# Performance work log

Measured on AMD Instinct MI355X. Metric: run time of the kernel, lower is better.

## Reference

```python
import jax, jax.numpy as jnp
import numpy as np

N_TOKEN = 267735
CUTS = [0, 20000, 40000, 200000, 267735]
DIV = 4
D_MODEL = 1024
N_HEAD = 16
D_HEAD = 64
D_INNER = 4096
N_LAYER = 4
QLEN = 512
MLEN = 512
BSZ = 4
EPS = 1e-5


def _ln(x, g, b):
    mu = jnp.mean(x, axis=-1, keepdims=True)
    var = jnp.var(x, axis=-1, keepdims=True)
    return (x - mu) * jax.lax.rsqrt(var + EPS) * g + b


def _rel_shift(x):
    # x: [qlen, klen, bsz, n_head]
    q, k, b, n = x.shape
    x = jnp.pad(x, ((0, 0), (1, 0), (0, 0), (0, 0)))
    x = x.reshape(k + 1, q, b, n)[1:]
    return x.reshape(q, k, b, n)


def setup_inputs() -> dict:
    key = jax.random.key(0)
    ks = list(jax.random.split(key, 32))
    p = lambda i, shape: 0.02 * jax.random.normal(ks[i], shape, dtype=jnp.float32)
    inp = {}
    inp['input_ids'] = jax.random.randint(ks[0], (BSZ, QLEN), 0, N_TOKEN, dtype=jnp.int32)
    inp['mems'] = 0.05 * jax.random.normal(ks[1], (N_LAYER, MLEN, BSZ, D_MODEL), dtype=jnp.float32)
    # adaptive embedding: cluster tables + projections (div_val=4)
    for i in range(4):
        l, r = CUTS[i], CUTS[i + 1]
        d_i = D_MODEL // (DIV ** i)
        inp[f'emb{i}'] = p(2 + i, (r - l, d_i))
        inp[f'proj{i}'] = p(6 + i, (d_i, D_MODEL))
    H = N_HEAD * D_HEAD
    inp['qkv_W'] = p(10, (N_LAYER, D_MODEL, 3 * H))
    inp['r_W'] = p(11, (N_LAYER, D_MODEL, H))
    inp['o_W'] = p(12, (N_LAYER, H, D_MODEL))
    inp['r_w_bias'] = p(13, (N_LAYER, N_HEAD, D_HEAD))
    inp['r_r_bias'] = p(14, (N_LAYER, N_HEAD, D_HEAD))
    inp['ln1_g'] = jnp.ones((N_LAYER, D_MODEL), jnp.float32)
    inp['ln1_b'] = jnp.zeros((N_LAYER, D_MODEL), jnp.float32)
    inp['ff_w1'] = p(15, (N_LAYER, D_MODEL, D_INNER))
    inp['ff_b1'] = jnp.zeros((N_LAYER, D_INNER), jnp.float32)
    inp['ff_w2'] = p(16, (N_LAYER, D_INNER, D_MODEL))
    inp['ff_b2'] = jnp.zeros((N_LAYER, D_MODEL), jnp.float32)
    inp['ln2_g'] = jnp.ones((N_LAYER, D_MODEL), jnp.float32)
    inp['ln2_b'] = jnp.zeros((N_LAYER, D_MODEL), jnp.float32)
    return inp


def _forward(input_ids, mems, embs, projs, qkv_W, r_W, o_W, r_w_bias, r_r_bias,
             ln1_g, ln1_b, ff_w1, ff_b1, ff_w2, ff_b2, ln2_g, ln2_b):
    ids = input_ids.T  # [qlen, bsz]
    qlen, bsz = ids.shape
    mems = jax.lax.stop_gradient(mems)  # mems are detached in the original
    mlen = mems.shape[1]
    klen = qlen + mlen

    # --- adaptive embedding (masked gather + scatter-add, same math as boolean_mask/scatter_nd) ---
    flat = ids.reshape(-1)
    emb = jnp.zeros((flat.shape[0], D_MODEL), jnp.float32)
    for i in range(4):
        l, r = CUTS[i], CUTS[i + 1]
        mask = (flat >= l) & (flat < r)
        idx = jnp.clip(flat - l, 0, r - l - 1)
        e_i = jnp.einsum('id,de->ie', embs[i][idx], projs[i])
        emb = emb + jnp.where(mask[:, None], e_i, 0.0)
    word_emb = (emb * (D_MODEL ** 0.5)).reshape(qlen, bsz, D_MODEL)

    # --- sinusoidal relative positions, pos_seq = klen-1 .. 0 ---
    pos_seq = jnp.arange(klen - 1, -1, -1, dtype=jnp.float32)
    inv_freq = 1.0 / (10000.0 ** (jnp.arange(0, D_MODEL, 2, dtype=jnp.float32) / D_MODEL))
    sinusoid = jnp.einsum('i,j->ij', pos_seq, inv_freq)
    pos_emb = jnp.concatenate([jnp.sin(sinusoid), jnp.cos(sinusoid)], axis=-1)  # [klen, d_model]

    # causal mask over memory-extended keys: [qlen, klen]
    attn_mask = jnp.triu(jnp.ones((qlen, klen), jnp.float32), k=1 + mlen)
    mask4 = attn_mask[:, :, None, None]
    scale = 1.0 / (D_HEAD ** 0.5)

    h = word_emb
    for l in range(N_LAYER):
        cat = jnp.concatenate([mems[l], h], axis=0)  # [klen, bsz, d_model]
        w_heads = jnp.einsum('kbd,dh->kbh', cat, qkv_W[l])
        r_head_k = jnp.einsum('kd,dh->kh', pos_emb, r_W[l]).reshape(klen, N_HEAD, D_HEAD)
        q_h, k_h, v_h = jnp.split(w_heads, 3, axis=-1)
        q_h = q_h[-qlen:].reshape(qlen, bsz, N_HEAD, D_HEAD)
        k_h = k_h.reshape(klen, bsz, N_HEAD, D_HEAD)
        v_h = v_h.reshape(klen, bsz, N_HEAD, D_HEAD)
        AC = jnp.einsum('ibnd,jbnd->ijbn', q_h + r_w_bias[l], k_h)
        BD = _rel_shift(jnp.einsum('ibnd,jnd->ijbn', q_h + r_r_bias[l], r_head_k))
        score = (AC + BD) * scale
        score = score * (1.0 - mask4) - 1e30 * mask4
        prob = jax.nn.softmax(score, axis=1)
        attn_vec = jnp.einsum('ijbn,jbnd->ibnd', prob, v_h).reshape(qlen, bsz, N_HEAD * D_HEAD)
        attn_out = jnp.einsum('ibh,hd->ibd', attn_vec, o_W[l])
        h = _ln(h + attn_out, ln1_g[l], ln1_b[l])
        ff = jnp.einsum('ibf,fd->ibd', jax.nn.relu(jnp.einsum('ibd,df->ibf', h, ff_w1[l]) + ff_b1[l]), ff_w2[l]) + ff_b2[l]
        h = _ln(h + ff, ln2_g[l], ln2_b[l])

    return h.transpose(1, 0, 2)  # [bsz, qlen, d_model]


def reference(input_ids, mems, emb0, emb1, emb2, emb3, proj0, proj1, proj2, proj3,
              qkv_W, r_W, o_W, r_w_bias, r_r_bias, ln1_g, ln1_b,
              ff_w1, ff_b1, ff_w2, ff_b2, ln2_g, ln2_b):
    return _forward(input_ids, mems, (emb0, emb1, emb2, emb3), (proj0, proj1, proj2, proj3),
                    qkv_W, r_W, o_W, r_w_bias, r_r_bias, ln1_g, ln1_b,
                    ff_w1, ff_b1, ff_w2, ff_b2, ln2_g, ln2_b)
```

## Files before the change

kernel.cpp:

```cpp
#include <hip/hip_runtime.h>

typedef __attribute__((ext_vector_type(8))) short bf16x8;
typedef __attribute__((ext_vector_type(4))) float f32x4;

#define N_LAYER 4
#define QLEN 512
#define MLEN 512
#define KLEN 1024
#define BSZ 4
#define DM 1024
#define NH 16
#define DH 64
#define DINNER 4096
#define EK 1408

__device__ __forceinline__ unsigned short f2bf(float x) {
    unsigned u = __float_as_uint(x);
    u += 0x7fffu + ((u >> 16) & 1u);
    return (unsigned short)(u >> 16);
}
__device__ __forceinline__ float bf2f(unsigned short v) {
    return __uint_as_float(((unsigned)v) << 16);
}

__device__ __forceinline__ void gload16(const unsigned short* g, unsigned short* l) {
    __builtin_amdgcn_global_load_lds(
        (const __attribute__((address_space(1))) unsigned int*)g,
        (__attribute__((address_space(3))) unsigned int*)l, 16, 0, 0);
}

__device__ __forceinline__ bf16x8 lds_read8_sw(const unsigned short* base, int row, int cb) {
    return *(const bf16x8*)((const char*)base + row * 128 + (cb ^ ((row & 7) << 4)));
}

__global__ __launch_bounds__(256)
void transpose_all(const float* __restrict__ qkvWl, const float* __restrict__ rWl,
                   const float* __restrict__ oWl, const float* __restrict__ w1l,
                   const float* __restrict__ w2l,
                   unsigned short* __restrict__ qkvT, unsigned short* __restrict__ rT,
                   unsigned short* __restrict__ oT, unsigned short* __restrict__ w1T,
                   unsigned short* __restrict__ w2T) {
    __shared__ float tile[32][33];
    int id = blockIdx.x;
    const float* W; unsigned short* D; int K, N, bx, by;
    if (id < 3072)      { W = qkvWl; D = qkvT; K = 1024; N = 3072; bx = id % 96;  by = id / 96; }
    else if (id < 4096) { id -= 3072; W = rWl;  D = rT;  K = 1024; N = 1024; bx = id & 31; by = id >> 5; }
    else if (id < 5120) { id -= 4096; W = oWl;  D = oT;  K = 1024; N = 1024; bx = id & 31; by = id >> 5; }
    else if (id < 9216) { id -= 5120; W = w1l;  D = w1T; K = 1024; N = 4096; bx = id & 127; by = id >> 7; }
    else                { id -= 9216; W = w2l;  D = w2T; K = 4096; N = 1024; bx = id & 31; by = id >> 5; }
    const int tx = threadIdx.x & 31, ty = threadIdx.x >> 5;
#pragma unroll
    for (int i = 0; i < 4; ++i)
        tile[ty + i * 8][tx] = W[(size_t)(by * 32 + ty + i * 8) * N + bx * 32 + tx];
    __syncthreads();
#pragma unroll
    for (int i = 0; i < 4; ++i)
        D[(size_t)(bx * 32 + ty + i * 8) * K + by * 32 + tx] = f2bf(tile[tx][ty + i * 8]);
}

__global__ __launch_bounds__(256)
void transpose_pad(const float* __restrict__ W, unsigned short* __restrict__ dst,
                   int K, int N, int dstLD, int dstOff) {
    __shared__ float tile[32][33];
    const int tx = threadIdx.x & 31, ty = threadIdx.x >> 5;
    const int bx = blockIdx.x, by = blockIdx.y;
#pragma unroll
    for (int i = 0; i < 4; ++i) {
        int k = by * 32 + ty + i * 8;
        tile[ty + i * 8][tx] = (k < K) ? W[(size_t)k * N + bx * 32 + tx] : 0.f;
    }
    __syncthreads();
#pragma unroll
    for (int i = 0; i < 4; ++i) {
        int n = bx * 32 + ty + i * 8;
        int k = by * 32 + tx;
        dst[(size_t)n * dstLD + dstOff + k] = f2bf(tile[tx][ty + i * 8]);
    }
}

__global__ __launch_bounds__(256)
void emb_gather(const int* __restrict__ ids,
                const float* __restrict__ e0, const float* __restrict__ e1,
                const float* __restrict__ e2, const float* __restrict__ e3,
                unsigned short* __restrict__ embA) {
    const int chunk = blockIdx.x * 256 + threadIdx.x;
    if (chunk >= 2048 * 176) return;
    const int t = chunk / 176;
    const int e8 = (chunk - t * 176) * 8;
    const int i = t >> 2, b = t & 3;
    const int id = ids[b * QLEN + i];
    const float* src = nullptr;
    if (e8 < 1024) {
        if (id < 20000) src = e0 + (size_t)id * 1024 + e8;
    } else if (e8 < 1280) {
        if (id >= 20000 && id < 40000) src = e1 + (size_t)(id - 20000) * 256 + (e8 - 1024);
    } else if (e8 < 1344) {
        if (id >= 40000 && id < 200000) src = e2 + (size_t)(id - 40000) * 64 + (e8 - 1280);
    } else if (e8 < 1360) {
        if (id >= 200000) src = e3 + (size_t)(id - 200000) * 16 + (e8 - 1344);
    }
    uint4 o = {0u, 0u, 0u, 0u};
    if (src) {
        float4 v0 = *(const float4*)src;
        float4 v1 = *(const float4*)(src + 4);
        o.x = (unsigned)f2bf(v0.x * 32.f) | ((unsigned)f2bf(v0.y * 32.f) << 16);
        o.y = (unsigned)f2bf(v0.z * 32.f) | ((unsigned)f2bf(v0.w * 32.f) << 16);
        o.z = (unsigned)f2bf(v1.x * 32.f) | ((unsigned)f2bf(v1.y * 32.f) << 16);
        o.w = (unsigned)f2bf(v1.z * 32.f) | ((unsigned)f2bf(v1.w * 32.f) << 16);
    }
    *(uint4*)(embA + (size_t)t * EK + e8) = o;
}

template <int MODE, int BN>
__global__ __launch_bounds__(256)
void gemm_bt(const unsigned short* __restrict__ A, const unsigned short* __restrict__ BT,
             float* __restrict__ C, unsigned short* __restrict__ Cbf,
             const float* __restrict__ bias,
             const float* __restrict__ rwb, const float* __restrict__ rrb,
             unsigned short* __restrict__ Qw, unsigned short* __restrict__ Qr,
             unsigned short* __restrict__ Kb, unsigned short* __restrict__ VTb,
             int M, int N, int K) {
    constexpr int NF = BN / 32;
    __shared__ unsigned short lA[2][128 * 64];
    __shared__ unsigned short lB[2][BN * 64];
    const int tid = threadIdx.x;
    const int w = tid >> 6, l = tid & 63;
    const int lane15 = l & 15, lh = l >> 4;
    const int nwg = gridDim.x;
    const int cpx = nwg >> 3;
    const int swz = (blockIdx.x & 7) * cpx + (blockIdx.x >> 3);
    const int nbn = N / BN;
    const int bm = swz / nbn, bn = swz % nbn;
    const int wr = (w >> 1) * 64, wc = (w & 1) * (BN / 2);

    f32x4 acc[4][NF] = {};

    const unsigned short* gA = A + (size_t)(bm * 128) * K;
    const unsigned short* gB = BT + (size_t)(bn * BN) * K;

    auto stage = [&](int buf, int k0) {
#pragma unroll
        for (int s = 0; s < 4; ++s) {
            int g = tid + s * 256, row = g >> 3;
            gload16(gA + (size_t)row * K + k0 + ((g & 7) ^ (row & 7)) * 8,
                    lA[buf] + g * 8);
        }
#pragma unroll
        for (int s = 0; s < BN / 32; ++s) {
            int g = tid + s * 256, row = g >> 3;
            gload16(gB + (size_t)row * K + k0 + ((g & 7) ^ (row & 7)) * 8,
                    lB[buf] + g * 8);
        }
    };

    stage(0, 0);
    __syncthreads();
    int cur = 0;
    for (int k0 = 0; k0 < K; k0 += 64) {
        if (k0 + 64 < K) stage(cur ^ 1, k0 + 64);
        const unsigned short* cA = lA[cur];
        const unsigned short* cB = lB[cur];
#pragma unroll
        for (int kk = 0; kk < 2; ++kk) {
            bf16x8 af[4], bfr[NF];
#pragma unroll
            for (int f = 0; f < 4; ++f)
                af[f] = lds_read8_sw(cA, wr + f * 16 + lane15, kk * 64 + lh * 16);
#pragma unroll
            for (int f = 0; f < NF; ++f)
                bfr[f] = lds_read8_sw(cB, wc + f * 16 + lane15, kk * 64 + lh * 16);
#pragma unroll
            for (int mi = 0; mi < 4; ++mi)
#pragma unroll
                for (int ni = 0; ni < NF; ++ni)
                    acc[mi][ni] = __builtin_amdgcn_mfma_f32_16x16x32_bf16(
                        af[mi], bfr[ni], acc[mi][ni], 0, 0, 0);
        }
        __syncthreads();
        cur ^= 1;
    }

#pragma unroll
    for (int mi = 0; mi < 4; ++mi) {
        int rowb = bm * 128 + wr + mi * 16 + lh * 4;
#pragma unroll
        for (int ni = 0; ni < NF; ++ni) {
            int col = bn * BN + wc + ni * 16 + lane15;
#pragma unroll
            for (int r = 0; r < 4; ++r) {
                float x = acc[mi][ni][r];
                if (MODE == 0) {
                    C[(size_t)(rowb + r) * N + col] = x;
                } else if (MODE == 1) {
                    x += bias[col];
                    Cbf[(size_t)(rowb + r) * N + col] = f2bf(x > 0.f ? x : 0.f);
                } else if (MODE == 2) {
                    C[(size_t)(rowb + r) * N + col] = x + bias[col];
                } else if (MODE == 3) {
                    int j = rowb >> 2;
                    int bb_ = r;
                    if (col < 1024) {
                        if (j >= MLEN) {
                            int i = j - MLEN, n = col >> 6, d = col & 63;
                            size_t o = ((size_t)(bb_ * NH + n) * QLEN + i) * DH + d;
                            Qw[o] = f2bf(x + rwb[col]);
                            Qr[o] = f2bf(x + rrb[col]);
                        }
                    } else if (col < 2048) {
                        int c2 = col - 1024, n = c2 >> 6, d = c2 & 63;
                        Kb[((size_t)(bb_ * NH + n) * KLEN + j) * DH + d] = f2bf(x);
                    } else {
                        int c2 = col - 2048, n = c2 >> 6, d = c2 & 63;
                        VTb[((size_t)(bb_ * NH + n) * DH + d) * KLEN + j] = f2bf(x);
                    }
                } else {
                    int j = rowb + r;
                    int n = col >> 6, d = col & 63;
                    Kb[((size_t)n * KLEN + j) * DH + d] = f2bf(x);
                }
            }
        }
    }
}

__global__ __launch_bounds__(256)
void pos_kernel(unsigned short* __restrict__ posbf) {
    const int p = blockIdx.x, tid = threadIdx.x;
    const float ps = (float)(KLEN - 1 - p);
    const float c = -2.0f * 9.210340371976184f / 1024.0f;
#pragma unroll
    for (int j4 = 0; j4 < 4; ++j4) {
        int j = tid + j4 * 256;
        int m = (j < 512) ? j : j - 512;
        float freq = __expf((float)m * c);
        float ang = ps * freq;
        float v = (j < 512) ? sinf(ang) : cosf(ang);
        posbf[(size_t)p * DM + j] = f2bf(v);
    }
}

__global__ __launch_bounds__(256)
void cat_kernel(const float* __restrict__ mem_l, const float* __restrict__ h,
                unsigned short* __restrict__ catbf) {
    const int t = blockIdx.x, tid = threadIdx.x;
    const float* src = (t < 2048) ? (mem_l + (size_t)t * DM) : (h + (size_t)(t - 2048) * DM);
    float4 v = ((const float4*)src)[tid];
    uint2 o;
    o.x = (unsigned)f2bf(v.x) | ((unsigned)f2bf(v.y) << 16);
    o.y = (unsigned)f2bf(v.z) | ((unsigned)f2bf(v.w) << 16);
    ((uint2*)(catbf + (size_t)t * DM))[tid] = o;
}

__global__ __launch_bounds__(64)
void attn_part(const unsigned short* __restrict__ Qw, const unsigned short* __restrict__ Qr,
               const unsigned short* __restrict__ Kb, const unsigned short* __restrict__ VTb,
               const unsigned short* __restrict__ Rb,
               unsigned short* __restrict__ Opart, float* __restrict__ ms) {
    __shared__ float lBD[16 * 83];
    __shared__ unsigned short lP[16 * 64];

    const int l = threadIdx.x;
    const int lane15 = l & 15, lh = l >> 4;
    const int blk = blockIdx.x;
    const int bn = blk & 63;
    const int rest = blk >> 6;
    const int rg = rest & 3;
    const int c = rest >> 2;

    const int n = bn & 15, b = bn >> 4;

    const int offt[8] = {0, 3, 7, 11, 15, 20, 25, 30};
    const int nctt[8] = {3, 4, 4, 4, 5, 5, 5, 6};
    int it = 0;
#pragma unroll
    for (int i = 1; i < 8; ++i) if (c >= offt[i]) it = i;
    const int cl = c - offt[it];
    const int nck = nctt[it];
    const int ntiles = it + 9;
    const int jt0 = (cl * ntiles) / nck;
    const int jt1 = ((cl + 1) * ntiles) / nck;
    const int i0 = it * 64;
    const int rowl = rg * 16 + lh * 4;

    bf16x8 qw[2], qr[2];
    {
        size_t qb = ((size_t)bn * QLEN + i0 + rg * 16 + lane15) * DH + lh * 8;
        qw[0] = *(const bf16x8*)(Qw + qb);
        qw[1] = *(const bf16x8*)(Qw + qb + 32);
        qr[0] = *(const bf16x8*)(Qr + qb);
        qr[1] = *(const bf16x8*)(Qr + qb + 32);
    }

    const unsigned short* kp = Kb + (size_t)bn * KLEN * DH + (size_t)(jt0 * 64 + lane15) * DH + lh * 8;
    const unsigned short* vp = VTb + (size_t)bn * DH * KLEN + (size_t)lane15 * KLEN + jt0 * 64 + lh * 8;
    const unsigned short* Rh = Rb + (size_t)n * KLEN * DH;

    f32x4 oacc[4] = {};
    float mrow[4], srow[4];
#pragma unroll
    for (int r = 0; r < 4; ++r) { mrow[r] = -1e30f; srow[r] = 0.f; }

    for (int jt = jt0; jt < jt1; ++jt) {
        bf16x8 kf[2][4], rf[2][5];
#pragma unroll
        for (int f = 0; f < 4; ++f) {
            const unsigned short* p = kp + (size_t)(f * 16) * DH;
            kf[0][f] = *(const bf16x8*)p;
            kf[1][f] = *(const bf16x8*)(p + 32);
        }
        const int rbase = 496 + 64 * (jt - it) - 16 * rg + lane15;
#pragma unroll
        for (int f = 0; f < 5; ++f) {
            int rr = rbase + 16 * f;
            if (rr > 1023) rr = 1023;
            const unsigned short* p = Rh + (size_t)rr * DH + lh * 8;
            rf[0][f] = *(const bf16x8*)p;
            rf[1][f] = *(const bf16x8*)(p + 32);
        }

        f32x4 sac[4] = {};
        f32x4 bd[5] = {};
        __builtin_amdgcn_s_setprio(1);
#pragma unroll
        for (int kk = 0; kk < 2; ++kk) {
#pragma unroll
            for (int f = 0; f < 4; ++f)
                sac[f] = __builtin_amdgcn_mfma_f32_16x16x32_bf16(qw[kk], kf[kk][f], sac[f], 0, 0, 0);
#pragma unroll
            for (int f = 0; f < 5; ++f)
                bd[f] = __builtin_amdgcn_mfma_f32_16x16x32_bf16(qr[kk], rf[kk][f], bd[f], 0, 0, 0);
        }
        __builtin_amdgcn_s_setprio(0);

#pragma unroll
        for (int f = 0; f < 5; ++f)
#pragma unroll
            for (int r = 0; r < 4; ++r)
                lBD[(lh * 4 + r) * 83 + lane15 + 16 * f] = bd[f][r];

        float pv[4][4];
        float tmax[4] = {-1e30f, -1e30f, -1e30f, -1e30f};
        const bool lastTile = (jt == it + 8);
#pragma unroll
        for (int f = 0; f < 4; ++f) {
            int lj = lane15 + 16 * f;
#pragma unroll
            for (int r = 0; r < 4; ++r) {
                int cc = 15 + lj - lh * 4 - r;
                float s = (sac[f][r] + lBD[(lh * 4 + r) * 83 + cc]) * 0.125f;
                if (lastTile && (lj > rowl + r)) s = -1e30f;
                pv[f][r] = s;
                tmax[r] = fmaxf(tmax[r], s);
            }
        }
#pragma unroll
        for (int off = 1; off < 16; off <<= 1)
#pragma unroll
            for (int r = 0; r < 4; ++r)
                tmax[r] = fmaxf(tmax[r], __shfl_xor(tmax[r], off));

        bf16x8 vf[2][4];
#pragma unroll
        for (int kk = 0; kk < 2; ++kk)
#pragma unroll
            for (int f = 0; f < 4; ++f)
                vf[kk][f] = *(const bf16x8*)(vp + (size_t)(f * 16) * KLEN + kk * 32);

        bool grow = false;
#pragma unroll
        for (int r = 0; r < 4; ++r) grow = grow || (tmax[r] > mrow[r] + 8.f);
        if (__any(grow)) {
#pragma unroll
            for (int r = 0; r < 4; ++r) {
                float nm = fmaxf(mrow[r], tmax[r]);
                float sc = __expf(mrow[r] - nm);
                mrow[r] = nm;
                srow[r] *= sc;
#pragma unroll
                for (int f = 0; f < 4; ++f) oacc[f][r] *= sc;
            }
        }
        float tsum[4];
#pragma unroll
        for (int r = 0; r < 4; ++r) {
            float ts = 0.f;
#pragma unroll
            for (int f = 0; f < 4; ++f) {
                float e = __expf(pv[f][r] - mrow[r]);
                pv[f][r] = e;
                ts += e;
            }
            tsum[r] = ts;
        }
#pragma unroll
        for (int off = 1; off < 16; off <<= 1)
#pragma unroll
            for (int r = 0; r < 4; ++r)
                tsum[r] += __shfl_xor(tsum[r], off);
#pragma unroll
        for (int r = 0; r < 4; ++r) srow[r] += tsum[r];

#pragma unroll
        for (int f = 0; f < 4; ++f)
#pragma unroll
            for (int r = 0; r < 4; ++r) {
                int row = lh * 4 + r, cb2 = (lane15 + 16 * f) * 2;
                *(unsigned short*)((char*)lP + row * 128 + (cb2 ^ ((row & 7) << 4))) =
                    f2bf(pv[f][r]);
            }
        bf16x8 pa[2];
        pa[0] = lds_read8_sw(lP, lane15, lh * 16);
        pa[1] = lds_read8_sw(lP, lane15, 64 + lh * 16);

        __builtin_amdgcn_s_setprio(1);
#pragma unroll
        for (int kk = 0; kk < 2; ++kk)
#pragma unroll
            for (int f = 0; f < 4; ++f)
                oacc[f] = __builtin_amdgcn_mfma_f32_16x16x32_bf16(pa[kk], vf[kk][f], oacc[f], 0, 0, 0);
        __builtin_amdgcn_s_setprio(0);

        kp += 64 * DH;
        vp += 64;
    }

    const int slot = (bn * 8 + it) * 6 + cl;
    unsigned short* Op = Opart + (size_t)slot * 4096;
#pragma unroll
    for (int f = 0; f < 4; ++f)
#pragma unroll
        for (int r = 0; r < 4; ++r)
            Op[(rowl + r) * 64 + lane15 + 16 * f] = f2bf(oacc[f][r]);
    if (lane15 == 0) {
        float* msp = ms + (size_t)slot * 128;
#pragma unroll
        for (int r = 0; r < 4; ++r) {
            msp[rowl + r] = mrow[r];
            msp[64 + rowl + r] = srow[r];
        }
    }
}

__global__ __launch_bounds__(256)
void attn_merge(const unsigned short* __restrict__ Opart, const float* __restrict__ ms,
                unsigned short* __restrict__ avec) {
    const int blk = blockIdx.x;
    const int bn = blk & 63, it = blk >> 6;
    const int n = bn & 15, b = bn >> 4;
    const int nctt[8] = {3, 4, 4, 4, 5, 5, 5, 6};
    const int k = nctt[it];
    const int tid = threadIdx.x;
    const int r = tid >> 2, cq = (tid & 3) * 16;
    const int base_slot = (bn * 8 + it) * 6;

    float a[6], s[6];
    float M = -1e30f;
    for (int c = 0; c < 6; ++c) {
        if (c < k) {
            a[c] = ms[(size_t)(base_slot + c) * 128 + r];
            s[c] = ms[(size_t)(base_slot + c) * 128 + 64 + r];
            M = fmaxf(M, a[c]);
        } else { a[c] = -1e30f; s[c] = 0.f; }
    }
    float S = 0.f;
    for (int c = 0; c < 6; ++c) {
        a[c] = (c < k) ? __expf(a[c] - M) : 0.f;
        S += s[c] * a[c];
    }
    float acc[16];
#pragma unroll
    for (int j = 0; j < 16; ++j) acc[j] = 0.f;
    for (int c = 0; c < k; ++c) {
        const bf16x8* op = (const bf16x8*)(Opart + (size_t)(base_slot + c) * 4096 + r * 64 + cq);
        bf16x8 v0 = op[0], v1 = op[1];
        float ac = a[c];
#pragma unroll
        for (int j = 0; j < 8; ++j) {
            acc[j]     += ac * bf2f((unsigned short)v0[j]);
            acc[8 + j] += ac * bf2f((unsigned short)v1[j]);
        }
    }
    float inv = 1.0f / S;
    int t = (it * 64 + r) * 4 + b;
    unsigned short* dst = avec + (size_t)t * DM + n * 64 + cq;
#pragma unroll
    for (int j = 0; j < 16; ++j) dst[j] = f2bf(acc[j] * inv);
}

__global__ __launch_bounds__(256)
void ln_kernel(const float* __restrict__ hin, const float* __restrict__ res,
               const float* __restrict__ g, const float* __restrict__ bb,
               float* __restrict__ hout, unsigned short* __restrict__ hbf) {
    __shared__ float ls[8];
    const int t = blockIdx.x, tid = threadIdx.x;
    float4 x = ((const float4*)(hin + (size_t)t * DM))[tid];
    float4 rr = ((const float4*)(res + (size_t)t * DM))[tid];
    float v0 = x.x + rr.x, v1 = x.y + rr.y, v2 = x.z + rr.z, v3 = x.w + rr.w;
    float s = v0 + v1 + v2 + v3;
    float sq = v0 * v0 + v1 * v1 + v2 * v2 + v3 * v3;
#pragma unroll
    for (int off = 1; off < 64; off <<= 1) {
        s += __shfl_xor(s, off);
        sq += __shfl_xor(sq, off);
    }
    const int w = tid >> 6;
    if ((tid & 63) == 0) { ls[w] = s; ls[4 + w] = sq; }
    __syncthreads();
    s = ls[0] + ls[1] + ls[2] + ls[3];
    sq = ls[4] + ls[5] + ls[6] + ls[7];
    float mu = s * (1.f / 1024.f);
    float var = sq * (1.f / 1024.f) - mu * mu;
    float rstd = rsqrtf(var + 1e-5f);
    float y[4] = {v0, v1, v2, v3};
    float4 of;
    uint2 ob;
    float* op = &of.x;
#pragma unroll
    for (int j = 0; j < 4; ++j) {
        int d = tid * 4 + j;
        op[j] = (y[j] - mu) * rstd * g[d] + bb[d];
    }
    ob.x = (unsigned)f2bf(of.x) | ((unsigned)f2bf(of.y) << 16);
    ob.y = (unsigned)f2bf(of.z) | ((unsigned)f2bf(of.w) << 16);
    ((float4*)(hout + (size_t)t * DM))[tid] = of;
    ((uint2*)(hbf + (size_t)t * DM))[tid] = ob;
}

__global__ __launch_bounds__(256)
void out_kernel(const float* __restrict__ h, float* __restrict__ out) {
    const int t = blockIdx.x, tid = threadIdx.x;
    const int i = t >> 2, b = t & 3;
    ((float4*)(out + ((size_t)b * QLEN + i) * DM))[tid] =
        ((const float4*)(h + (size_t)t * DM))[tid];
}

extern "C" void kernel_launch(void* const* d_in, const int* in_sizes, int n_in,
                              void* d_out, int out_size, void* d_ws, size_t ws_size,
                              hipStream_t stream) {
    const int* ids = (const int*)d_in[0];
    const float* mems = (const float*)d_in[1];
    const float* embp[4] = {nullptr, nullptr, nullptr, nullptr};
    const float* projp[4] = {nullptr, nullptr, nullptr, nullptr};
    const long long esz[4] = {20000LL * 1024, 20000LL * 256, 160000LL * 64, 67735LL * 16};
    const long long psz[4] = {1024LL * 1024, 256LL * 1024, 64LL * 1024, 16LL * 1024};
    for (int idx = 2; idx <= 9 && idx < n_in; ++idx) {
        long long s = in_sizes[idx];
        for (int c = 0; c < 4; ++c) {
            if (s == esz[c]) embp[c] = (const float*)d_in[idx];
            else if (s == psz[c]) projp[c] = (const float*)d_in[idx];
        }
    }
    const float* qkvW = (const float*)d_in[10];
    const float* rW   = (const float*)d_in[11];
    const float* oW   = (const float*)d_in[12];
    const float* rwb  = (const float*)d_in[13];
    const float* rrb  = (const float*)d_in[14];
    const float* ln1g = (const float*)d_in[15];
    const float* ln1b = (const float*)d_in[16];
    const float* ffw1 = (const float*)d_in[17];
    const float* ffb1 = (const float*)d_in[18];
    const float* ffw2 = (const float*)d_in[19];
    const float* ffb2 = (const float*)d_in[20];
    const float* ln2g = (const float*)d_in[21];
    const float* ln2b = (const float*)d_in[22];

    size_t off = 0;
    char* base = (char*)d_ws;
    auto alloc = [&](size_t bytes) -> char* {
        char* p = base + off;
        off = (off + bytes + 255) & ~(size_t)255;
        return p;
    };
    unsigned short* qkvT  = (unsigned short*)alloc(3072ull * 1024 * 2);
    unsigned short* rT    = (unsigned short*)alloc(1024ull * 1024 * 2);
    unsigned short* oT    = (unsigned short*)alloc(1024ull * 1024 * 2);
    unsigned short* w1T   = (unsigned short*)alloc(4096ull * 1024 * 2);
    unsigned short* w2T   = (unsigned short*)alloc(1024ull * 4096 * 2);
    unsigned short* embA  = (unsigned short*)alloc(2048ull * EK * 2);
    unsigned short* embBT = (unsigned short*)alloc(1024ull * EK * 2);
    float* h              = (float*)alloc(2048ull * 1024 * 4);
    unsigned short* hbf   = (unsigned short*)alloc(2048ull * 1024 * 2);
    unsigned short* catb  = (unsigned short*)alloc(4096ull * 1024 * 2);
    unsigned short* posb  = (unsigned short*)alloc(1024ull * 1024 * 2);
    unsigned short* Qw    = (unsigned short*)alloc(4ull * 16 * 512 * 64 * 2);
    unsigned short* Qr    = (unsigned short*)alloc(4ull * 16 * 512 * 64 * 2);
    unsigned short* Kb    = (unsigned short*)alloc(4ull * 16 * 1024 * 64 * 2);
    unsigned short* VTb   = (unsigned short*)alloc(4ull * 16 * 1024 * 64 * 2);
    unsigned short* Rb    = (unsigned short*)alloc(16ull * 1024 * 64 * 2);
    unsigned short* avec  = (unsigned short*)alloc(2048ull * 1024 * 2);
    float* resid          = (float*)alloc(2048ull * 1024 * 4);
    unsigned short* ff1b  = (unsigned short*)alloc(2048ull * 4096 * 2);
    unsigned short* Opart = (unsigned short*)alloc(3072ull * 4096 * 2);
    float* msbuf          = (float*)alloc(3072ull * 128 * 4);
    (void)ws_size; (void)out_size;

    emb_gather<<<(2048 * 176 + 255) / 256, 256, 0, stream>>>(
        ids, embp[0], embp[1], embp[2], embp[3], embA);
    transpose_pad<<<dim3(32, 32), 256, 0, stream>>>(projp[0], embBT, 1024, 1024, EK, 0);
    transpose_pad<<<dim3(32, 8),  256, 0, stream>>>(projp[1], embBT, 256,  1024, EK, 1024);
    transpose_pad<<<dim3(32, 2),  256, 0, stream>>>(projp[2], embBT, 64,   1024, EK, 1280);
    transpose_pad<<<dim3(32, 2),  256, 0, stream>>>(projp[3], embBT, 16,   1024, EK, 1344);
    pos_kernel<<<1024, 256, 0, stream>>>(posb);
    gemm_bt<0, 128><<<(2048 / 128) * (1024 / 128), 256, 0, stream>>>(
        embA, embBT, h, nullptr, nullptr, nullptr, nullptr, nullptr, nullptr, nullptr, nullptr,
        2048, 1024, EK);

    for (int l = 0; l < N_LAYER; ++l) {
        const float* qkvWl = qkvW + (size_t)l * 1024 * 3072;
        const float* rWl   = rW + (size_t)l * 1024 * 1024;
        const float* oWl   = oW + (size_t)l * 1024 * 1024;
        const float* w1l   = ffw1 + (size_t)l * 1024 * 4096;
        const float* w2l   = ffw2 + (size_t)l * 4096 * 1024;

        transpose_all<<<13312, 256, 0, stream>>>(qkvWl, rWl, oWl, w1l, w2l,
                                                 qkvT, rT, oT, w1T, w2T);

        cat_kernel<<<4096, 256, 0, stream>>>(mems + (size_t)l * 2048 * 1024, h, catb);

        gemm_bt<3, 128><<<(4096 / 128) * (3072 / 128), 256, 0, stream>>>(
            catb, qkvT, nullptr, nullptr, nullptr,
            rwb + l * 1024, rrb + l * 1024, Qw, Qr, Kb, VTb, 4096, 3072, 1024);

        gemm_bt<4, 64><<<(1024 / 128) * (1024 / 64), 256, 0, stream>>>(
            posb, rT, nullptr, nullptr, nullptr,
            nullptr, nullptr, nullptr, nullptr, Rb, nullptr, 1024, 1024, 1024);

        attn_part<<<64 * 144, 64, 0, stream>>>(Qw, Qr, Kb, VTb, Rb, Opart, msbuf);
        attn_merge<<<512, 256, 0, stream>>>(Opart, msbuf, avec);

        gemm_bt<0, 64><<<(2048 / 128) * (1024 / 64), 256, 0, stream>>>(
            avec, oT, resid, nullptr, nullptr, nullptr, nullptr, nullptr, nullptr, nullptr, nullptr,
            2048, 1024, 1024);
        ln_kernel<<<2048, 256, 0, stream>>>(h, resid, ln1g + l * 1024, ln1b + l * 1024, h, hbf);

        gemm_bt<1, 128><<<(2048 / 128) * (4096 / 128), 256, 0, stream>>>(
            hbf, w1T, nullptr, ff1b, ffb1 + l * 4096, nullptr, nullptr, nullptr, nullptr, nullptr, nullptr,
            2048, 4096, 1024);
        gemm_bt<2, 64><<<(2048 / 128) * (1024 / 64), 256, 0, stream>>>(
            ff1b, w2T, resid, nullptr, ffb2 + l * 1024, nullptr, nullptr, nullptr, nullptr, nullptr, nullptr,
            2048, 1024, 4096);
        ln_kernel<<<2048, 256, 0, stream>>>(h, resid, ln2g + l * 1024, ln2b + l * 1024, h, hbf);
    }

    out_kernel<<<2048, 256, 0, stream>>>(h, (float*)d_out);
}
```

Baseline: 1.180 ms.

## Precompute relative-position BD scores in a separate GEMM before attention

```diff
diff --git a/kernel.cpp b/kernel.cpp
--- a/kernel.cpp
+++ b/kernel.cpp
@@ -13,6 +13,7 @@
 #define DH 64
 #define DINNER 4096
 #define EK 1408
+#define BDLD 1152
 
 __device__ __forceinline__ unsigned short f2bf(float x) {
     unsigned u = __float_as_uint(x);
@@ -224,6 +225,60 @@
 }
 
 __global__ __launch_bounds__(256)
+void bd_gemm(const unsigned short* __restrict__ Qr, const unsigned short* __restrict__ Rb,
+             unsigned short* __restrict__ BDs) {
+    __shared__ unsigned short lA[128 * 64];
+    __shared__ unsigned short lB[128 * 64];
+    const int tid = threadIdx.x;
+    const int w = tid >> 6, l = tid & 63;
+    const int lane15 = l & 15, lh = l >> 4;
+    const int blk = blockIdx.x;
+    const int bn = blk & 63;
+    const int tile = blk >> 6;
+    const int mi_ = tile & 3, nj = tile >> 2;
+    const int n = bn & 15;
+    const int wr = (w >> 1) * 64, wc = (w & 1) * 64;
+
+    const unsigned short* gA = Qr + (size_t)bn * QLEN * DH + (size_t)(mi_ * 128) * 64;
+    const unsigned short* gB = Rb + (size_t)n * KLEN * DH + (size_t)(nj * 128) * 64;
+#pragma unroll
+    for (int s = 0; s < 4; ++s) {
+        int g = tid + s * 256, row = g >> 3;
+        gload16(gA + (size_t)row * 64 + ((g & 7) ^ (row & 7)) * 8, lA + g * 8);
+        gload16(gB + (size_t)row * 64 + ((g & 7) ^ (row & 7)) * 8, lB + g * 8);
+    }
+    __syncthreads();
+    f32x4 acc[4][4] = {};
+#pragma unroll
+    for (int kk = 0; kk < 2; ++kk) {
+        bf16x8 af[4], bfr[4];
+#pragma unroll
+        for (int f = 0; f < 4; ++f) {
+            af[f]  = lds_read8_sw(lA, wr + f * 16 + lane15, kk * 64 + lh * 16);
+            bfr[f] = lds_read8_sw(lB, wc + f * 16 + lane15, kk * 64 + lh * 16);
+        }
+#pragma unroll
+        for (int mi = 0; mi < 4; ++mi)
+#pragma unroll
+            for (int ni = 0; ni < 4; ++ni)
+                acc[mi][ni] = __builtin_amdgcn_mfma_f32_16x16x32_bf16(
+                    af[mi], bfr[ni], acc[mi][ni], 0, 0, 0);
+    }
+    unsigned short* out = BDs + (size_t)bn * 512 * BDLD;
+#pragma unroll
+    for (int mi = 0; mi < 4; ++mi) {
+        int rowb = mi_ * 128 + wr + mi * 16 + lh * 4;
+#pragma unroll
+        for (int ni = 0; ni < 4; ++ni) {
+            int col = nj * 128 + wc + ni * 16 + lane15;
+#pragma unroll
+            for (int r = 0; r < 4; ++r)
+                out[(size_t)(rowb + r) * BDLD + col] = f2bf(acc[mi][ni][r]);
+        }
+    }
+}
+
+__global__ __launch_bounds__(256)
 void pos_kernel(unsigned short* __restrict__ posbf) {
     const int p = blockIdx.x, tid = threadIdx.x;
     const float ps = (float)(KLEN - 1 - p);
@@ -254,9 +309,8 @@
 __global__ __launch_bounds__(64)
 void attn_part(const unsigned short* __restrict__ Qw, const unsigned short* __restrict__ Qr,
                const unsigned short* __restrict__ Kb, const unsigned short* __restrict__ VTb,
-               const unsigned short* __restrict__ Rb,
+               const unsigned short* __restrict__ BDs,
                unsigned short* __restrict__ Opart, float* __restrict__ ms) {
-    __shared__ float lBD[16 * 83];
     __shared__ unsigned short lP[16 * 64];
 
     const int l = threadIdx.x;
@@ -266,8 +320,6 @@
     const int rest = blk >> 6;
     const int rg = rest & 3;
     const int c = rest >> 2;
-
-    const int n = bn & 15, b = bn >> 4;
 
     const int offt[8] = {0, 3, 7, 11, 15, 20, 25, 30};
     const int nctt[8] = {3, 4, 4, 4, 5, 5, 5, 6};
@@ -282,18 +334,22 @@
     const int i0 = it * 64;
     const int rowl = rg * 16 + lh * 4;
 
-    bf16x8 qw[2], qr[2];
+    bf16x8 qw[2];
     {
         size_t qb = ((size_t)bn * QLEN + i0 + rg * 16 + lane15) * DH + lh * 8;
         qw[0] = *(const bf16x8*)(Qw + qb);
         qw[1] = *(const bf16x8*)(Qw + qb + 32);
-        qr[0] = *(const bf16x8*)(Qr + qb);
-        qr[1] = *(const bf16x8*)(Qr + qb + 32);
     }
 
     const unsigned short* kp = Kb + (size_t)bn * KLEN * DH + (size_t)(jt0 * 64 + lane15) * DH + lh * 8;
     const unsigned short* vp = VTb + (size_t)bn * DH * KLEN + (size_t)lane15 * KLEN + jt0 * 64 + lh * 8;
-    const unsigned short* Rh = Rb + (size_t)n * KLEN * DH;
+    const unsigned short* bdp[4];
+#pragma unroll
+    for (int r = 0; r < 4; ++r) {
+        int row = i0 + rowl + r;
+        bdp[r] = BDs + (size_t)bn * 512 * BDLD + (size_t)row * BDLD
+                 + (511 - row) + jt0 * 64 + lane15;
+    }
 
     f32x4 oacc[4] = {};
     float mrow[4], srow[4];
@@ -301,42 +357,29 @@
     for (int r = 0; r < 4; ++r) { mrow[r] = -1e30f; srow[r] = 0.f; }
 
     for (int jt = jt0; jt < jt1; ++jt) {
-        bf16x8 kf[2][4], rf[2][5];
+        float bdv[4][4];
+#pragma unroll
+        for (int f = 0; f < 4; ++f)
+#pragma unroll
+            for (int r = 0; r < 4; ++r)
+                bdv[f][r] = bf2f(bdp[r][16 * f]);
+
+        bf16x8 kf[2][4];
 #pragma unroll
         for (int f = 0; f < 4; ++f) {
             const unsigned short* p = kp + (size_t)(f * 16) * DH;
             kf[0][f] = *(const bf16x8*)p;
             kf[1][f] = *(const bf16x8*)(p + 32);
         }
-        const int rbase = 496 + 64 * (jt - it) - 16 * rg + lane15;
-#pragma unroll
-        for (int f = 0; f < 5; ++f) {
-            int rr = rbase + 16 * f;
-            if (rr > 1023) rr = 1023;
-            const unsigned short* p = Rh + (size_t)rr * DH + lh * 8;
-            rf[0][f] = *(const bf16x8*)p;
-            rf[1][f] = *(const bf16x8*)(p + 32);
-        }
 
         f32x4 sac[4] = {};
-        f32x4 bd[5] = {};
         __builtin_amdgcn_s_setprio(1);
 #pragma unroll
-        for (int kk = 0; kk < 2; ++kk) {
+        for (int kk = 0; kk < 2; ++kk)
 #pragma unroll
             for (int f = 0; f < 4; ++f)
                 sac[f] = __builtin_amdgcn_mfma_f32_16x16x32_bf16(qw[kk], kf[kk][f], sac[f], 0, 0, 0);
-#pragma unroll
-            for (int f = 0; f < 5; ++f)
-                bd[f] = __builtin_amdgcn_mfma_f32_16x16x32_bf16(qr[kk], rf[kk][f], bd[f], 0, 0, 0);
-        }
         __builtin_amdgcn_s_setprio(0);
-
-#pragma unroll
-        for (int f = 0; f < 5; ++f)
-#pragma unroll
-            for (int r = 0; r < 4; ++r)
-                lBD[(lh * 4 + r) * 83 + lane15 + 16 * f] = bd[f][r];
 
         float pv[4][4];
         float tmax[4] = {-1e30f, -1e30f, -1e30f, -1e30f};
@@ -346,8 +389,7 @@
             int lj = lane15 + 16 * f;
 #pragma unroll
             for (int r = 0; r < 4; ++r) {
-                int cc = 15 + lj - lh * 4 - r;
-                float s = (sac[f][r] + lBD[(lh * 4 + r) * 83 + cc]) * 0.125f;
+                float s = (sac[f][r] + bdv[f][r]) * 0.125f;
                 if (lastTile && (lj > rowl + r)) s = -1e30f;
                 pv[f][r] = s;
                 tmax[r] = fmaxf(tmax[r], s);
@@ -422,6 +464,8 @@
 
         kp += 64 * DH;
         vp += 64;
+#pragma unroll
+        for (int r = 0; r < 4; ++r) bdp[r] += 64;
     }
 
     const int slot = (bn * 8 + it) * 6 + cl;
@@ -592,6 +636,7 @@
     unsigned short* ff1b  = (unsigned short*)alloc(2048ull * 4096 * 2);
     unsigned short* Opart = (unsigned short*)alloc(3072ull * 4096 * 2);
     float* msbuf          = (float*)alloc(3072ull * 128 * 4);
+    unsigned short* BDs   = (unsigned short*)alloc(64ull * 512 * BDLD * 2);
     (void)ws_size; (void)out_size;
 
     emb_gather<<<(2048 * 176 + 255) / 256, 256, 0, stream>>>(
@@ -625,7 +670,9 @@
             posb, rT, nullptr, nullptr, nullptr,
             nullptr, nullptr, nullptr, nullptr, Rb, nullptr, 1024, 1024, 1024);
 
-        attn_part<<<64 * 144, 64, 0, stream>>>(Qw, Qr, Kb, VTb, Rb, Opart, msbuf);
+        bd_gemm<<<64 * 32, 256, 0, stream>>>(Qr, Rb, BDs);
+
+        attn_part<<<64 * 144, 64, 0, stream>>>(Qw, Qr, Kb, VTb, BDs, Opart, msbuf);
         attn_merge<<<512, 256, 0, stream>>>(Opart, msbuf, avec);
 
         gemm_bt<0, 64><<<(2048 / 128) * (1024 / 64), 256, 0, stream>>>(
```

Result: faster. 1.141 ms (-3.3%).
